# Optimization experiments

Measured on AMD Instinct MI355X. Metric: run time of the kernel, lower is better.

Reference implementation:

```python
import jax, jax.numpy as jnp
import numpy as np

PATCH_LENGTH = 200

def setup_inputs() -> dict:
    key = jax.random.key(0)
    eeg_input = jax.random.normal(key, (16, 32, 1000, 64), dtype=jnp.float32)
    return {"eeg_input": eeg_input}

def reference(eeg_input):
    # eeg_input: [B, W, T, C]
    B, W, T, C = eeg_input.shape
    nt = T // PATCH_LENGTH  # number of time patches per channel
    T_used = nt * PATCH_LENGTH
    # Torch loops iterate ch_idx (outer), t_idx (inner) -> channel-major patch order.
    # [B, W, T, C] -> [B, W, C, T] -> [B, W, C, nt, P] -> [B, W, C*nt, P]
    x = jnp.transpose(eeg_input[:, :, :T_used, :], (0, 1, 3, 2))
    patches = x.reshape(B, W, C * nt, PATCH_LENGTH)
    channel_indices = jnp.repeat(jnp.arange(C, dtype=jnp.int64), nt)  # [C*nt]
    time_indices = jnp.tile(jnp.arange(nt, dtype=jnp.int64), C)       # [C*nt]
    return patches, channel_indices, time_indices
```

## Files before the change

kernel.cpp:

```cpp
#include <hip/hip_runtime.h>


#define TDIM 1000
#define CDIM 64
#define TT   100
#define LSTR 65
#define NTILE 10
#define PATCH_ELEMS 32768000

__global__ __launch_bounds__(256) void labram_patcher_kernel(
    const float* __restrict__ in, float* __restrict__ out)
{
    __shared__ float lds[TT * LSTR];

    const int tid  = threadIdx.x;
    const int tile = blockIdx.x % NTILE;
    const int bw   = blockIdx.x / NTILE;
    const int t0   = tile * TT;

    const float4* in4 = (const float4*)in + (size_t)(bw * TDIM + t0) * (CDIM / 4);
    for (int i = tid; i < TT * 16; i += 256) {
        int ti = i >> 4;
        int c4 = i & 15;
        float4 v = in4[ti * 16 + c4];
        int base = ti * LSTR + c4 * 4;
        lds[base + 0] = v.x;
        lds[base + 1] = v.y;
        lds[base + 2] = v.z;
        lds[base + 3] = v.w;
    }
    __syncthreads();

    for (int i = tid; i < CDIM * 25; i += 256) {
        int c  = i / 25;
        int j  = i - c * 25;
        int ti = j * 4;
        float4 v;
        v.x = lds[(ti + 0) * LSTR + c];
        v.y = lds[(ti + 1) * LSTR + c];
        v.z = lds[(ti + 2) * LSTR + c];
        v.w = lds[(ti + 3) * LSTR + c];
        size_t off = (size_t)(bw * CDIM + c) * TDIM + (t0 + ti);
        *(float4*)(out + off) = v;
    }

    if (blockIdx.x == 0) {
        for (int i = tid; i < 320; i += 256) {
            out[PATCH_ELEMS + i]       = (float)(i / 5);
            out[PATCH_ELEMS + 320 + i] = (float)(i % 5);
        }
    }
}

extern "C" void kernel_launch(void* const* d_in, const int* in_sizes, int n_in,
                              void* d_out, int out_size, void* d_ws, size_t ws_size,
                              hipStream_t stream) {
    const float* in = (const float*)d_in[0];
    float* out = (float*)d_out;
    dim3 grid(512 * NTILE);
    dim3 block(256);
    labram_patcher_kernel<<<grid, block, 0, stream>>>(in, out);
}
```

Measured before the change: 249.5 us.

## Tile transpose by channel quarters with XOR-swizzled LDS and full-row stores

Changes the transpose tiling from 100-timestep tiles over all 64 channels to 16-channel groups covering the full 1000-timestep range, with 512-thread blocks. All global loads are issued into registers before the LDS writes, and the LDS uses an XOR swizzle in place of padding to avoid bank conflicts. Each output channel row is then written as one contiguous 4 KB run with scalar coalesced stores. The cost is larger LDS per block (64 KB), which can lower occupancy, plus scalar 4-byte stores and input reads of only 64 bytes per row.

```diff
diff --git a/kernel.cpp b/kernel.cpp
--- a/kernel.cpp
+++ b/kernel.cpp
@@ -3,52 +3,65 @@
 
 #define TDIM 1000
 #define CDIM 64
-#define TT   100
-#define LSTR 65
-#define NTILE 10
+#define CQ   16
+#define NCQ  4
 #define PATCH_ELEMS 32768000
 
-__global__ __launch_bounds__(256) void labram_patcher_kernel(
+__global__ __launch_bounds__(512) void labram_patcher_kernel(
     const float* __restrict__ in, float* __restrict__ out)
 {
-    __shared__ float lds[TT * LSTR];
+    __shared__ float lds[TDIM * CQ];
 
-    const int tid  = threadIdx.x;
-    const int tile = blockIdx.x % NTILE;
-    const int bw   = blockIdx.x / NTILE;
-    const int t0   = tile * TT;
+    const int tid = threadIdx.x;
+    const int cq  = blockIdx.x & (NCQ - 1);
+    const int bw  = blockIdx.x >> 2;
 
-    const float4* in4 = (const float4*)in + (size_t)(bw * TDIM + t0) * (CDIM / 4);
-    for (int i = tid; i < TT * 16; i += 256) {
-        int ti = i >> 4;
-        int c4 = i & 15;
-        float4 v = in4[ti * 16 + c4];
-        int base = ti * LSTR + c4 * 4;
-        lds[base + 0] = v.x;
-        lds[base + 1] = v.y;
-        lds[base + 2] = v.z;
-        lds[base + 3] = v.w;
+    const float4* gsrc = (const float4*)(in + (size_t)bw * (TDIM * CDIM) + cq * CQ);
+
+    float4 v[8];
+    #pragma unroll
+    for (int k = 0; k < 7; ++k) {
+        const int i = tid + k * 512;
+        v[k] = gsrc[(i >> 2) * 16 + (i & 3)];
+    }
+    const int i7 = tid + 7 * 512;
+    if (i7 < 4000)
+        v[7] = gsrc[(i7 >> 2) * 16 + (i7 & 3)];
+
+    #pragma unroll
+    for (int k = 0; k < 8; ++k) {
+        const int i = tid + k * 512;
+        if (k < 7 || i < 4000) {
+            const int t = i >> 2;
+            const int u = i & 3;
+            const int s = (t >> 1) & 15;
+            const int b = t * CQ;
+            lds[b + ((u * 4 + 0) ^ s)] = v[k].x;
+            lds[b + ((u * 4 + 1) ^ s)] = v[k].y;
+            lds[b + ((u * 4 + 2) ^ s)] = v[k].z;
+            lds[b + ((u * 4 + 3) ^ s)] = v[k].w;
+        }
     }
     __syncthreads();
 
-    for (int i = tid; i < CDIM * 25; i += 256) {
-        int c  = i / 25;
-        int j  = i - c * 25;
-        int ti = j * 4;
-        float4 v;
-        v.x = lds[(ti + 0) * LSTR + c];
-        v.y = lds[(ti + 1) * LSTR + c];
-        v.z = lds[(ti + 2) * LSTR + c];
-        v.w = lds[(ti + 3) * LSTR + c];
-        size_t off = (size_t)(bw * CDIM + c) * TDIM + (t0 + ti);
-        *(float4*)(out + off) = v;
+    const int w = tid >> 6;
+    const int l = tid & 63;
+    float* dst = out + (size_t)bw * (CDIM * TDIM) + cq * (CQ * TDIM);
+
+    #pragma unroll
+    for (int rr = 0; rr < 2; ++rr) {
+        const int r = w * 2 + rr;
+        #pragma unroll
+        for (int tb = 0; tb < TDIM; tb += 64) {
+            const int t = tb + l;
+            if (t < TDIM)
+                dst[r * TDIM + t] = lds[t * CQ + (r ^ ((t >> 1) & 15))];
+        }
     }
 
-    if (blockIdx.x == 0) {
-        for (int i = tid; i < 320; i += 256) {
-            out[PATCH_ELEMS + i]       = (float)(i / 5);
-            out[PATCH_ELEMS + 320 + i] = (float)(i % 5);
-        }
+    if (blockIdx.x == 0 && tid < 320) {
+        out[PATCH_ELEMS + tid]       = (float)(tid / 5);
+        out[PATCH_ELEMS + 320 + tid] = (float)(tid % 5);
     }
 }
 
@@ -57,7 +70,7 @@
                               hipStream_t stream) {
     const float* in = (const float*)d_in[0];
     float* out = (float*)d_out;
-    dim3 grid(512 * NTILE);
-    dim3 block(256);
+    dim3 grid(512 * NCQ);
+    dim3 block(512);
     labram_patcher_kernel<<<grid, block, 0, stream>>>(in, out);
 }
```

Result: faster. 232.5 us (-6.8%).

## Tile transpose by 4-channel groups over full time axis with XCD-aware block remap

Applied to the files above, without the earlier changes.

Each block now takes one (batch,window) slice and a group of 4 channels across all 1000 time steps, instead of a 100-step tile across all 64 channels. It loads strided float4 values holding 4 channels per timestep, stores them channel-major in LDS, and writes 4 contiguous 4000-byte output rows with float4 stores. Block indices are remapped so that consecutive blocks on the same XCD handle neighbouring channel groups, which is meant to improve L2 reuse of the partially read input rows. The trade-off is that each global read is a 16-byte access at a 256-byte stride, so input reads are less coalesced, with more blocks in flight via launch_bounds occupancy 8.

```diff
diff --git a/kernel.cpp b/kernel.cpp
--- a/kernel.cpp
+++ b/kernel.cpp
@@ -2,49 +2,52 @@
 
 
 #define TDIM 1000
-#define CDIM 64
-#define TT   100
-#define LSTR 65
-#define NTILE 10
 #define PATCH_ELEMS 32768000
 
-__global__ __launch_bounds__(256) void labram_patcher_kernel(
+__global__ __launch_bounds__(256, 8) void labram_patcher_kernel(
     const float* __restrict__ in, float* __restrict__ out)
 {
-    __shared__ float lds[TT * LSTR];
+    __shared__ float lds[4 * TDIM];
 
     const int tid  = threadIdx.x;
-    const int tile = blockIdx.x % NTILE;
-    const int bw   = blockIdx.x / NTILE;
-    const int t0   = tile * TT;
+    const int phys = blockIdx.x;
+    const int virt = (phys & 7) * 1024 + (phys >> 3);
+    const int bw = virt >> 4;
+    const int cq = virt & 15;
 
-    const float4* in4 = (const float4*)in + (size_t)(bw * TDIM + t0) * (CDIM / 4);
-    for (int i = tid; i < TT * 16; i += 256) {
-        int ti = i >> 4;
-        int c4 = i & 15;
-        float4 v = in4[ti * 16 + c4];
-        int base = ti * LSTR + c4 * 4;
-        lds[base + 0] = v.x;
-        lds[base + 1] = v.y;
-        lds[base + 2] = v.z;
-        lds[base + 3] = v.w;
+    const float4* gsrc = (const float4*)in + (size_t)bw * 16000 + cq;
+
+    float4 v[4];
+    #pragma unroll
+    for (int k = 0; k < 3; ++k)
+        v[k] = gsrc[(size_t)(tid + k * 256) * 16];
+    const int t3 = tid + 768;
+    if (t3 < TDIM)
+        v[3] = gsrc[(size_t)t3 * 16];
+
+    #pragma unroll
+    for (int k = 0; k < 4; ++k) {
+        const int t = tid + k * 256;
+        if (k < 3 || t < TDIM) {
+            lds[            t] = v[k].x;
+            lds[    TDIM +  t] = v[k].y;
+            lds[2 * TDIM +  t] = v[k].z;
+            lds[3 * TDIM +  t] = v[k].w;
+        }
     }
     __syncthreads();
 
-    for (int i = tid; i < CDIM * 25; i += 256) {
-        int c  = i / 25;
-        int j  = i - c * 25;
-        int ti = j * 4;
-        float4 v;
-        v.x = lds[(ti + 0) * LSTR + c];
-        v.y = lds[(ti + 1) * LSTR + c];
-        v.z = lds[(ti + 2) * LSTR + c];
-        v.w = lds[(ti + 3) * LSTR + c];
-        size_t off = (size_t)(bw * CDIM + c) * TDIM + (t0 + ti);
-        *(float4*)(out + off) = v;
+    const float4* lds4 = (const float4*)lds;
+    float4* dst = (float4*)out + (size_t)bw * 16000 + (size_t)cq * 1000;
+
+    #pragma unroll
+    for (int k = 0; k < 4; ++k) {
+        const int i = tid + k * 256;
+        if (k < 3 || i < 1000)
+            dst[i] = lds4[i];
     }
 
-    if (blockIdx.x == 0) {
+    if (phys == 0) {
         for (int i = tid; i < 320; i += 256) {
             out[PATCH_ELEMS + i]       = (float)(i / 5);
             out[PATCH_ELEMS + 320 + i] = (float)(i % 5);
@@ -57,7 +60,7 @@
                               hipStream_t stream) {
     const float* in = (const float*)d_in[0];
     float* out = (float*)d_out;
-    dim3 grid(512 * NTILE);
+    dim3 grid(512 * 16);
     dim3 block(256);
     labram_patcher_kernel<<<grid, block, 0, stream>>>(in, out);
 }
```

Measured after the change: 241.1 us. -3.3%, faster.

## Replace LDS tile transpose with per-wave register 4x4 transposes

Applied to the files above, without the earlier changes.

The shared-memory staging and barrier are removed. Each wave now handles a 16-timestep by 64-channel tile: every thread loads four float4 rows and transposes them in registers into four float4 column stores. A fixed 2048-block grid walks the tiles with a grid-stride loop, and the last tile overlaps its neighbour to cover the ragged end. This removes LDS traffic and synchronisation, but each channel row is now written in 64-byte pieces instead of longer contiguous runs, which may reduce write coalescing.

```diff
diff --git a/kernel.cpp b/kernel.cpp
--- a/kernel.cpp
+++ b/kernel.cpp
@@ -1,51 +1,43 @@
 #include <hip/hip_runtime.h>
 
 
-#define TDIM 1000
-#define CDIM 64
-#define TT   100
-#define LSTR 65
-#define NTILE 10
 #define PATCH_ELEMS 32768000
+#define NTILES_T 63
+#define TOTAL_TILES (512 * NTILES_T)
 
 __global__ __launch_bounds__(256) void labram_patcher_kernel(
     const float* __restrict__ in, float* __restrict__ out)
 {
-    __shared__ float lds[TT * LSTR];
+    const int lane = threadIdx.x & 63;
+    const int tq   = lane >> 4;
+    const int cq   = lane & 15;
+    const int wid    = (blockIdx.x * 256 + threadIdx.x) >> 6;
+    const int nwaves = (gridDim.x * 256) >> 6;
 
-    const int tid  = threadIdx.x;
-    const int tile = blockIdx.x % NTILE;
-    const int bw   = blockIdx.x / NTILE;
-    const int t0   = tile * TT;
+    for (int tile = wid; tile < TOTAL_TILES; tile += nwaves) {
+        const int bw = tile / NTILES_T;
+        const int ti = tile - bw * NTILES_T;
+        const int t0 = (ti < 62) ? ti * 16 : 984;
+        const int tr = t0 + tq * 4;
 
-    const float4* in4 = (const float4*)in + (size_t)(bw * TDIM + t0) * (CDIM / 4);
-    for (int i = tid; i < TT * 16; i += 256) {
-        int ti = i >> 4;
-        int c4 = i & 15;
-        float4 v = in4[ti * 16 + c4];
-        int base = ti * LSTR + c4 * 4;
-        lds[base + 0] = v.x;
-        lds[base + 1] = v.y;
-        lds[base + 2] = v.z;
-        lds[base + 3] = v.w;
-    }
-    __syncthreads();
+        const float4* src = (const float4*)in
+                          + (size_t)bw * 16000 + (size_t)tr * 16 + cq;
+        const float4 r0 = src[0];
+        const float4 r1 = src[16];
+        const float4 r2 = src[32];
+        const float4 r3 = src[48];
 
-    for (int i = tid; i < CDIM * 25; i += 256) {
-        int c  = i / 25;
-        int j  = i - c * 25;
-        int ti = j * 4;
-        float4 v;
-        v.x = lds[(ti + 0) * LSTR + c];
-        v.y = lds[(ti + 1) * LSTR + c];
-        v.z = lds[(ti + 2) * LSTR + c];
-        v.w = lds[(ti + 3) * LSTR + c];
-        size_t off = (size_t)(bw * CDIM + c) * TDIM + (t0 + ti);
-        *(float4*)(out + off) = v;
+        float4* dst = (float4*)out
+                    + (size_t)bw * 16000 + (size_t)(cq * 4) * 250
+                    + (t0 >> 2) + tq;
+        dst[0]   = make_float4(r0.x, r1.x, r2.x, r3.x);
+        dst[250] = make_float4(r0.y, r1.y, r2.y, r3.y);
+        dst[500] = make_float4(r0.z, r1.z, r2.z, r3.z);
+        dst[750] = make_float4(r0.w, r1.w, r2.w, r3.w);
     }
 
     if (blockIdx.x == 0) {
-        for (int i = tid; i < 320; i += 256) {
+        for (int i = threadIdx.x; i < 320; i += 256) {
             out[PATCH_ELEMS + i]       = (float)(i / 5);
             out[PATCH_ELEMS + 320 + i] = (float)(i % 5);
         }
@@ -57,7 +49,7 @@
                               hipStream_t stream) {
     const float* in = (const float*)d_in[0];
     float* out = (float*)d_out;
-    dim3 grid(512 * NTILE);
+    dim3 grid(2048);
     dim3 block(256);
     labram_patcher_kernel<<<grid, block, 0, stream>>>(in, out);
 }
```

Measured after the change: 261.4 us. 4.8% more time.
